# Optimization experiments

Hardware: AMD Instinct MI355X
Metric: run time of the kernel (lower is better)

The kernel has to match this reference:

```python
import jax, jax.numpy as jnp
import numpy as np

N_MEL = 80
ATTN = 512
PRENET = 256
RNN = 1024
B, T = 32, 800


def setup_inputs() -> dict:
    key = jax.random.key(0)
    ks = jax.random.split(key, 10)
    s = lambda fan_in: 1.0 / np.sqrt(fan_in)
    return {
        "memory": jax.random.normal(ks[0], (B, T, ATTN), jnp.float32),
        "y_mels": jax.random.normal(ks[1], (B, T, N_MEL), jnp.float32),
        # Prenet: two bias-free linears with ReLU
        "prenet_w1": jax.random.uniform(ks[2], (PRENET, N_MEL), jnp.float32, -s(N_MEL), s(N_MEL)),
        "prenet_w2": jax.random.uniform(ks[3], (PRENET, PRENET), jnp.float32, -s(PRENET), s(PRENET)),
        # LSTM (1 layer): input dim = PRENET + ATTN = 768, gate order i,f,g,o
        "w_ih": jax.random.uniform(ks[4], (4 * RNN, PRENET + ATTN), jnp.float32, -s(RNN), s(RNN)),
        "w_hh": jax.random.uniform(ks[5], (4 * RNN, RNN), jnp.float32, -s(RNN), s(RNN)),
        "b_ih": jax.random.uniform(ks[6], (4 * RNN,), jnp.float32, -s(RNN), s(RNN)),
        "b_hh": jax.random.uniform(ks[7], (4 * RNN,), jnp.float32, -s(RNN), s(RNN)),
        # Linear projection: (RNN + ATTN) -> N_MEL, with bias
        "proj_w": jax.random.uniform(ks[8], (N_MEL, RNN + ATTN), jnp.float32, -s(RNN + ATTN), s(RNN + ATTN)),
        "proj_b": jax.random.uniform(ks[9], (N_MEL,), jnp.float32, -s(RNN + ATTN), s(RNN + ATTN)),
    }


def _decoder_fwd(memory, y_mels, prenet_w1, prenet_w2, w_ih, w_hh, b_ih, b_hh, proj_w, proj_b):
    b, t, _ = memory.shape
    # teacher-forced previous frames: step j consumes zeros (j=0) or y_mels[:, j-1]
    prev = jnp.concatenate([jnp.zeros((b, 1, N_MEL), memory.dtype), y_mels[:, : t - 1]], axis=1)  # [B,T,80]
    # prenet (eval mode: dropout off; double relu == relu)
    h = jax.nn.relu(jnp.einsum("btm,pm->btp", prev, prenet_w1))
    h = jax.nn.relu(jnp.einsum("btp,qp->btq", h, prenet_w2))  # [B,T,256]
    x = jnp.concatenate([h, memory], axis=-1)  # [B,T,768]
    # precompute input-to-gate contributions for all steps
    gates_in = jnp.einsum("btd,gd->tbg", x, w_ih) + (b_ih + b_hh)  # [T,B,4H]

    def step(carry, g_in):
        hh, cc = carry
        gates = g_in + hh @ w_hh.T  # [B,4H]
        i, f_, g, o = jnp.split(gates, 4, axis=-1)
        cc = jax.nn.sigmoid(f_) * cc + jax.nn.sigmoid(i) * jnp.tanh(g)
        hh = jax.nn.sigmoid(o) * jnp.tanh(cc)
        return (hh, cc), hh

    init = (jnp.zeros((b, RNN), memory.dtype), jnp.zeros((b, RNN), memory.dtype))
    _, hs = jax.lax.scan(step, init, gates_in)  # [T,B,H]
    hs = jnp.transpose(hs, (1, 0, 2))  # [B,T,H]
    out = jnp.concatenate([hs, memory], axis=-1)  # [B,T,H+ATTN]
    mel = jnp.einsum("btd,md->btm", out, proj_w) + proj_b  # [B,T,80]
    return mel.reshape(b, -1, N_MEL)


def reference(memory, y_mels, prenet_w1, prenet_w2, w_ih, w_hh, b_ih, b_hh, proj_w, proj_b):
    return _decoder_fwd(memory, y_mels, prenet_w1, prenet_w2, w_ih, w_hh, b_ih, b_hh, proj_w, proj_b)
```

## Files before the change

kernel.cpp:

```cpp
#include <hip/hip_runtime.h>
#include <hip/hip_bf16.h>

typedef unsigned short u16;
typedef unsigned int u32;
typedef unsigned long long u64;
typedef __attribute__((ext_vector_type(8))) short short8;
typedef __attribute__((ext_vector_type(4))) float f32x4;

#define ROWS 25600

__device__ __forceinline__ u16 f2bf(float f){
  u32 x = __builtin_bit_cast(u32, f);
  u32 r = (x + 0x7FFFu + ((x >> 16) & 1u)) >> 16;
  return (u16)r;
}
__device__ __forceinline__ float bf2f(u16 h){
  return __builtin_bit_cast(float, ((u32)h) << 16);
}
__device__ __forceinline__ float sigf(float x){
  x = fminf(fmaxf(x, -30.f), 30.f);
  return 1.f / (1.f + __expf(-x));
}
__device__ __forceinline__ float tanh_(float x){
  x = fminf(fmaxf(x, -15.f), 15.f);
  float e = __expf(-2.f * x);
  return (1.f - e) / (1.f + e);
}


__global__ void initk(u32* wflags, u32* pflags, u16* hb){
  int i = blockIdx.x * blockDim.x + threadIdx.x;
  int stride = blockDim.x * gridDim.x;
  for (int j = i; j < 64 * 32; j += stride) wflags[j] = 0;
  for (int j = i; j < 192 * 32; j += stride) pflags[j] = 0;
  for (int j = i; j < 2 * 32 * 1024; j += stride) hb[j] = 0;
}

__global__ void sentinel_fill(float* out, int n, float val){
  for (int i = blockIdx.x * blockDim.x + threadIdx.x; i < n;
       i += blockDim.x * gridDim.x)
    out[i] = val;
}

__global__ void prep_prev(const float* __restrict__ ym, u16* __restrict__ prevp){
  int idx = blockIdx.x * blockDim.x + threadIdx.x;
  if (idx >= ROWS * 96) return;
  int r = idx / 96, c = idx - r * 96;
  int b = r / 800, t = r - b * 800;
  float v = 0.f;
  if (c < 80 && t > 0) v = ym[(u64)(b * 800 + (t - 1)) * 80 + c];
  prevp[idx] = f2bf(v);
}

__global__ void prep_w(const float* __restrict__ w1, const float* __restrict__ w2,
                       const float* __restrict__ wih, const float* __restrict__ pw,
                       const float* __restrict__ bih, const float* __restrict__ bhh,
                       const float* __restrict__ whh,
                       u16* __restrict__ w1p, u16* __restrict__ w2b,
                       u16* __restrict__ wihb, u16* __restrict__ projp,
                       float* __restrict__ bsum, u16* __restrict__ whhb){
  int idx = blockIdx.x * blockDim.x + threadIdx.x;
  const int n1 = 256 * 96, n2 = 256 * 256, n3 = 4096 * 768, n4 = 128 * 1536, n5 = 4096;
  const int n6 = 4096 * 1024;
  if (idx < n1){
    int r = idx / 96, c = idx - r * 96;
    w1p[idx] = (c < 80) ? f2bf(w1[r * 80 + c]) : (u16)0;
  } else if ((idx -= n1) < n2){
    w2b[idx] = f2bf(w2[idx]);
  } else if ((idx -= n2) < n3){
    wihb[idx] = f2bf(wih[idx]);
  } else if ((idx -= n3) < n4){
    int r = idx / 1536;
    projp[idx] = (r < 80) ? f2bf(pw[idx]) : (u16)0;
  } else if ((idx -= n4) < n5){
    bsum[idx] = bih[idx] + bhh[idx];
  } else if ((idx -= n5) < n6){
    whhb[idx] = f2bf(whh[idx]);
  }
}


template<int RELU, int OUTF32, int HASBIAS, int AMAP, int SPLIT>
__global__ __launch_bounds__(256, 2) void gemm_tn(
    const u16* __restrict__ A, const float* __restrict__ A2,
    const u16* __restrict__ W, void* __restrict__ Cv,
    const float* __restrict__ bias,
    int M, int K, int lda, int lda2, int ldw, int ldc, int nmax,
    int ksplit, int t0)
{
  __shared__ __align__(16) u16 As[128 * 32];
  __shared__ __align__(16) u16 Ws[128 * 32];
  const int tid = threadIdx.x;
  const int lane = tid & 63;
  const int wv = tid >> 6;
  const int wr = wv & 1, wc = wv >> 1;
  const int mtiles = M >> 7;
  const int ntiles = gridDim.x / mtiles;
  int bm, bn;
  if (mtiles & 7){
    bm = blockIdx.x % mtiles;
    bn = blockIdx.x / mtiles;
  } else {
    int per = 8 * ntiles;
    int g = blockIdx.x / per, rem = blockIdx.x % per;
    bm = g * 8 + (rem & 7);
    bn = rem >> 3;
  }
  const int m0 = bm << 7, n0 = bn << 7;
  const int KT = K >> 5;

  f32x4 acc[4][4] = {};

  const int r0 = tid >> 2, c0 = tid & 3;
  const int r1 = r0 + 64;
  const u16* Wb = W + (u64)n0 * ldw;
  const int ws0 = r0 * 32 + ((c0 ^ ((r0 >> 1) & 3)) << 3);
  const int ws1 = r1 * 32 + ((c0 ^ ((r1 >> 1) & 3)) << 3);

  auto rowmap = [&](int r) -> int {
    int gr = m0 + r;
    if (AMAP) return (gr & 31) * 800 + t0 + (gr >> 5);
    return gr;
  };
  const u64 ab0 = (u64)rowmap(r0) * lda;
  const u64 ab1 = (u64)rowmap(r1) * lda;
  const u64 af0 = SPLIT ? (u64)rowmap(r0) * lda2 : 0;
  const u64 af1 = SPLIT ? (u64)rowmap(r1) * lda2 : 0;

  auto aload = [&](u64 rb, u64 rf, int k) -> uint4 {
    if (SPLIT && k >= ksplit){
      const float* p = A2 + rf + (k - ksplit);
      const float4 a = *(const float4*)p;
      const float4 b = *(const float4*)(p + 4);
      uint4 r;
      r.x = (u32)f2bf(a.x) | ((u32)f2bf(a.y) << 16);
      r.y = (u32)f2bf(a.z) | ((u32)f2bf(a.w) << 16);
      r.z = (u32)f2bf(b.x) | ((u32)f2bf(b.y) << 16);
      r.w = (u32)f2bf(b.z) | ((u32)f2bf(b.w) << 16);
      return r;
    }
    return *(const uint4*)(A + rb + k);
  };

  uint4 ra0 = aload(ab0, af0, c0 * 8);
  uint4 ra1 = aload(ab1, af1, c0 * 8);
  uint4 rw0 = *(const uint4*)(Wb + r0 * ldw + c0 * 8);
  uint4 rw1 = *(const uint4*)(Wb + r1 * ldw + c0 * 8);

  const int r16 = lane & 15, cg = lane >> 4;

  for (int kt = 0; kt < KT; ++kt){
    *(uint4*)&As[ws0] = ra0;
    *(uint4*)&As[ws1] = ra1;
    *(uint4*)&Ws[ws0] = rw0;
    *(uint4*)&Ws[ws1] = rw1;
    __syncthreads();
    if (kt + 1 < KT){
      const int k0 = ((kt + 1) << 5) + c0 * 8;
      ra0 = aload(ab0, af0, k0);
      ra1 = aload(ab1, af1, k0);
      rw0 = *(const uint4*)(Wb + r0 * ldw + k0);
      rw1 = *(const uint4*)(Wb + r1 * ldw + k0);
    }
    short8 af[4], wf[4];
    #pragma unroll
    for (int mt = 0; mt < 4; ++mt){
      const int row = (wr << 6) + (mt << 4) + r16;
      af[mt] = *(const short8*)&As[(row << 5) + ((cg ^ ((row >> 1) & 3)) << 3)];
    }
    #pragma unroll
    for (int nt = 0; nt < 4; ++nt){
      const int row = (wc << 6) + (nt << 4) + r16;
      wf[nt] = *(const short8*)&Ws[(row << 5) + ((cg ^ ((row >> 1) & 3)) << 3)];
    }
    #pragma unroll
    for (int mt = 0; mt < 4; ++mt)
      #pragma unroll
      for (int nt = 0; nt < 4; ++nt)
        acc[mt][nt] = __builtin_amdgcn_mfma_f32_16x16x32_bf16(af[mt], wf[nt], acc[mt][nt], 0, 0, 0);
    __syncthreads();
  }

  #pragma unroll
  for (int nt = 0; nt < 4; ++nt){
    const int gn = n0 + (wc << 6) + (nt << 4) + r16;
    if (gn < nmax){
      float bv = 0.f;
      if (HASBIAS) bv = bias[gn];
      #pragma unroll
      for (int mt = 0; mt < 4; ++mt){
        #pragma unroll
        for (int r = 0; r < 4; ++r){
          const int gm = m0 + (wr << 6) + (mt << 4) + (cg << 2) + r;
          float v = acc[mt][nt][r] + bv;
          if (RELU) v = fmaxf(v, 0.f);
          if (OUTF32) ((float*)Cv)[(u64)gm * ldc + gn] = v;
          else        ((u16*)Cv)[(u64)gm * ldc + gn] = f2bf(v);
        }
      }
    }
  }
}


__shared__ __align__(16) u16 fs_hsm[32 * 1024];
__shared__ __align__(16) float fs_gsm[2048];
__shared__ __align__(16) u16 fs_As[128 * 32];
__shared__ __align__(16) u16 fs_Ws[128 * 32];

__device__ void gemm_tile_512(
    const u16* __restrict__ pn, const float* __restrict__ memory,
    const u16* __restrict__ wihb, const float* __restrict__ bsum,
    u16* __restrict__ slot, int bm, int bn, int t0)
{
  const int tid = threadIdx.x;
  const bool act = (tid < 256);
  const int lane = tid & 63;
  const int wv4 = (tid >> 6) & 3;
  const int wr = wv4 & 1, wc = wv4 >> 1;
  const int m0 = bm << 7, n0 = bn << 7;
  const int KT = 24;

  f32x4 acc[4][4] = {};
  const int r0 = tid >> 2, c0 = tid & 3;
  const int r1 = r0 + 64;
  const u16* Wb = wihb + (u64)n0 * 768;
  const int ws0 = r0 * 32 + ((c0 ^ ((r0 >> 1) & 3)) << 3);
  const int ws1 = r1 * 32 + ((c0 ^ ((r1 >> 1) & 3)) << 3);

  auto rowmap = [&](int r) -> int {
    int gr = m0 + r;
    return (gr & 31) * 800 + t0 + (gr >> 5);
  };
  u64 ab0 = 0, ab1 = 0, af0 = 0, af1 = 0;
  if (act){
    ab0 = (u64)rowmap(r0) * 256;  af0 = (u64)rowmap(r0) * 512;
    ab1 = (u64)rowmap(r1) * 256;  af1 = (u64)rowmap(r1) * 512;
  }
  auto aload = [&](u64 rb, u64 rf, int k) -> uint4 {
    if (k >= 256){
      const float* p = memory + rf + (k - 256);
      const float4 a = *(const float4*)p;
      const float4 b = *(const float4*)(p + 4);
      uint4 r;
      r.x = (u32)f2bf(a.x) | ((u32)f2bf(a.y) << 16);
      r.y = (u32)f2bf(a.z) | ((u32)f2bf(a.w) << 16);
      r.z = (u32)f2bf(b.x) | ((u32)f2bf(b.y) << 16);
      r.w = (u32)f2bf(b.z) | ((u32)f2bf(b.w) << 16);
      return r;
    }
    return *(const uint4*)(pn + rb + k);
  };

  uint4 ra0, ra1, rw0, rw1;
  if (act){
    ra0 = aload(ab0, af0, c0 * 8);
    ra1 = aload(ab1, af1, c0 * 8);
    rw0 = *(const uint4*)(Wb + r0 * 768 + c0 * 8);
    rw1 = *(const uint4*)(Wb + r1 * 768 + c0 * 8);
  }
  const int r16 = lane & 15, cg = lane >> 4;

  for (int kt = 0; kt < KT; ++kt){
    if (act){
      *(uint4*)&fs_As[ws0] = ra0;
      *(uint4*)&fs_As[ws1] = ra1;
      *(uint4*)&fs_Ws[ws0] = rw0;
      *(uint4*)&fs_Ws[ws1] = rw1;
    }
    __syncthreads();
    if (act){
      if (kt + 1 < KT){
        const int k0 = ((kt + 1) << 5) + c0 * 8;
        ra0 = aload(ab0, af0, k0);
        ra1 = aload(ab1, af1, k0);
        rw0 = *(const uint4*)(Wb + r0 * 768 + k0);
        rw1 = *(const uint4*)(Wb + r1 * 768 + k0);
      }
      short8 af[4], wf[4];
      #pragma unroll
      for (int mt = 0; mt < 4; ++mt){
        const int row = (wr << 6) + (mt << 4) + r16;
        af[mt] = *(const short8*)&fs_As[(row << 5) + ((cg ^ ((row >> 1) & 3)) << 3)];
      }
      #pragma unroll
      for (int nt = 0; nt < 4; ++nt){
        const int row = (wc << 6) + (nt << 4) + r16;
        wf[nt] = *(const short8*)&fs_Ws[(row << 5) + ((cg ^ ((row >> 1) & 3)) << 3)];
      }
      #pragma unroll
      for (int mt = 0; mt < 4; ++mt)
        #pragma unroll
        for (int nt = 0; nt < 4; ++nt)
          acc[mt][nt] = __builtin_amdgcn_mfma_f32_16x16x32_bf16(af[mt], wf[nt], acc[mt][nt], 0, 0, 0);
    }
    __syncthreads();
  }

  if (act){
    #pragma unroll
    for (int nt = 0; nt < 4; ++nt){
      const int gn = n0 + (wc << 6) + (nt << 4) + r16;
      const float bv = bsum[gn];
      #pragma unroll
      for (int mt = 0; mt < 4; ++mt){
        #pragma unroll
        for (int r = 0; r < 4; ++r){
          const int gm = m0 + (wr << 6) + (mt << 4) + (cg << 2) + r;
          slot[(u64)gm * 4096 + gn] = f2bf(acc[mt][nt][r] + bv);
        }
      }
    }
  }
}

__global__ __launch_bounds__(512, 1) void fused(
    const u16* __restrict__ whhb, const u16* __restrict__ pn,
    const float* __restrict__ memory, const u16* __restrict__ wihb,
    const float* __restrict__ bsum, u16* __restrict__ ring,
    u16* __restrict__ hb, u16* __restrict__ hs,
    u32* wflags, u32* pflags, int CT, int nchunks)
{
  const int tid = threadIdx.x;
  const int lane = tid & 63;
  const int wv = tid >> 6;
  const u64 deadline = __builtin_amdgcn_s_memrealtime() + 100000000ull;

  if (blockIdx.x >= 64){
    const int p = blockIdx.x - 64;
    for (int c = 0; c < nchunks; ++c){
      const int t0 = c * CT;
      const int steps = (800 - t0 < CT) ? (800 - t0) : CT;
      if (c >= 2){
        if (wv == 0){
          const u32 need = (u32)((c - 1) * CT);
          u32 it = 0;
          while (1){
            u32 v = __hip_atomic_load(&wflags[lane << 5], __ATOMIC_RELAXED,
                                      __HIP_MEMORY_SCOPE_AGENT);
            if (__all((int)(v >= need))) break;
            __builtin_amdgcn_s_sleep(8);
            if (((++it) & 15u) == 0u &&
                __builtin_amdgcn_s_memrealtime() > deadline) break;
          }
        }
        __syncthreads();
      }
      const int mt = (steps * 32) >> 7;
      const int TPC = mt * 32;
      u16* slot = ring + (u64)(c & 1) * ((u64)CT << 17);
      for (int tau = p; tau < TPC; tau += 192){
        gemm_tile_512(pn, memory, wihb, bsum, slot, tau % mt, tau / mt, t0);
      }
      __syncthreads();
      if (wv == 0){
        __builtin_amdgcn_fence(__ATOMIC_RELEASE, "agent");
        if (tid == 0)
          __hip_atomic_store(&pflags[p << 5], (u32)(c + 1), __ATOMIC_RELAXED,
                             __HIP_MEMORY_SCOPE_AGENT);
      }
    }
    return;
  }

  const int gate = wv & 3, mh = wv >> 2;
  const int u0 = blockIdx.x << 4;
  const int r16 = lane & 15, cg = lane >> 4;

  short8 wf[32];
  {
    const u16* wrow = whhb + (u64)((gate << 10) + u0 + r16) * 1024 + (cg << 3);
    #pragma unroll
    for (int kk = 0; kk < 32; ++kk)
      wf[kk] = *(const short8*)(wrow + (kk << 5));
  }

  const int pb = tid >> 4, pu = tid & 15;
  float ccell = 0.f;
  const int arow = (mh << 4) + r16;
  const u16* abase = &fs_hsm[arow << 10];
  const int aswz = (arow & 7) << 3;

  int c = 0, i = 0;
  for (int t = 0; t < 800; ++t, ++i){
    if (i == CT){ c++; i = 0; }
    const bool boundary = (i == 0);
    const u16* gslot = ring + (u64)(c & 1) * ((u64)CT << 17);
    const u64 gb = ((u64)i * 32 + pb) * 4096 + u0 + pu;
    const int cur = t & 1;

    u16 gv0 = 0, gv1 = 0, gv2 = 0, gv3 = 0;
    if (!boundary){
      gv0 = gslot[gb];        gv1 = gslot[gb + 1024];
      gv2 = gslot[gb + 2048]; gv3 = gslot[gb + 3072];
    }
    if (boundary || t > 0){
      if (wv == 0){
        if (boundary){
          const u32 need = (u32)(c + 1);
          u32 it = 0;
          while (1){
            u32 a = __hip_atomic_load(&pflags[lane << 5], __ATOMIC_RELAXED,
                                      __HIP_MEMORY_SCOPE_AGENT);
            u32 b = __hip_atomic_load(&pflags[(lane + 64) << 5], __ATOMIC_RELAXED,
                                      __HIP_MEMORY_SCOPE_AGENT);
            u32 d = __hip_atomic_load(&pflags[(lane + 128) << 5], __ATOMIC_RELAXED,
                                      __HIP_MEMORY_SCOPE_AGENT);
            u32 m = a < b ? a : b; m = m < d ? m : d;
            if (__all((int)(m >= need))) break;
            if (((++it) & 15u) == 0u &&
                __builtin_amdgcn_s_memrealtime() > deadline) break;
          }
        }
        if (t > 0){
          u32 it = 0;
          while (1){
            u32 v = __hip_atomic_load(&wflags[lane << 5], __ATOMIC_RELAXED,
                                      __HIP_MEMORY_SCOPE_AGENT);
            if (__all((int)(v >= (u32)t))) break;
            if (((++it) & 15u) == 0u &&
                __builtin_amdgcn_s_memrealtime() > deadline) break;
          }
        }
        __builtin_amdgcn_fence(__ATOMIC_ACQUIRE, "agent");
      }
      __syncthreads();
    }
    if (boundary){
      gv0 = gslot[gb];        gv1 = gslot[gb + 1024];
      gv2 = gslot[gb + 2048]; gv3 = gslot[gb + 3072];
    }
    {
      const u16* hsrc = hb + cur * 32768;
      uint4 hr[8];
      #pragma unroll
      for (int j = 0; j < 8; ++j) hr[j] = *(const uint4*)(hsrc + (((j << 9) + tid) << 3));
      #pragma unroll
      for (int j = 0; j < 8; ++j){
        const int ci = (j << 9) + tid;
        const int row = ci >> 7, k16 = ci & 127;
        *(uint4*)&fs_hsm[(row << 10) + ((k16 ^ (row & 7)) << 3)] = hr[j];
      }
    }
    __syncthreads();
    f32x4 acc = {};
    #pragma unroll
    for (int kk = 0; kk < 32; ++kk){
      const int k16 = (kk << 2) + cg;
      const short8 af = *(const short8*)&abase[((k16 << 3) ^ aswz)];
      acc = __builtin_amdgcn_mfma_f32_16x16x32_bf16(af, wf[kk], acc, 0, 0, 0);
    }
    #pragma unroll
    for (int r = 0; r < 4; ++r){
      const int m = (mh << 4) + (cg << 2) + r;
      fs_gsm[(gate << 9) + (m << 4) + r16] = acc[r];
    }
    __syncthreads();
    {
      const int o = (pb << 4) + pu;
      const float gi = fs_gsm[o]        + bf2f(gv0);
      const float gf = fs_gsm[512 + o]  + bf2f(gv1);
      const float gg = fs_gsm[1024 + o] + bf2f(gv2);
      const float go = fs_gsm[1536 + o] + bf2f(gv3);
      ccell = sigf(gf) * ccell + sigf(gi) * tanh_(gg);
      const float h = sigf(go) * tanh_(ccell);
      const u16 hbits = f2bf(h);
      hs[(((u64)pb * 800 + t) << 10) + u0 + pu] = hbits;
      const u32 other = (u32)(u16)__shfl_xor((int)(u32)hbits, 1);
      if ((tid & 1) == 0){
        const u32 w = ((u32)hbits) | (other << 16);
        u32* dst = (u32*)(void*)hb + ((cur ^ 1) * 16384 + (pb << 9) + (u0 >> 1) + (pu >> 1));
        __hip_atomic_store(dst, w, __ATOMIC_RELAXED, __HIP_MEMORY_SCOPE_AGENT);
      }
    }
    __syncthreads();
    if (tid == 0)
      __hip_atomic_store(&wflags[blockIdx.x << 5], (u32)(t + 1), __ATOMIC_RELAXED,
                         __HIP_MEMORY_SCOPE_AGENT);
  }
}


extern "C" void kernel_launch(void* const* d_in, const int* in_sizes, int n_in,
                              void* d_out, int out_size, void* d_ws, size_t ws_size,
                              hipStream_t stream){
  const float* memory = (const float*)d_in[0];
  const float* ymels  = (const float*)d_in[1];
  const float* w1     = (const float*)d_in[2];
  const float* w2     = (const float*)d_in[3];
  const float* wih    = (const float*)d_in[4];
  const float* whh    = (const float*)d_in[5];
  const float* bih    = (const float*)d_in[6];
  const float* bhh    = (const float*)d_in[7];
  const float* pw     = (const float*)d_in[8];
  const float* pbias  = (const float*)d_in[9];
  float* out = (float*)d_out;

  char* ws = (char*)d_ws;
  u64 off = 0;
  auto alloc = [&](u64 bytes) -> void* {
    void* p = ws + off;
    off += (bytes + 255) & ~255ull;
    return p;
  };
  u16* hs    = (u16*)alloc((u64)ROWS * 1024 * 2);
  u16* pn    = (u16*)alloc((u64)ROWS * 256 * 2);
  u16* wihb  = (u16*)alloc((u64)4096 * 768 * 2);
  u16* whhb  = (u16*)alloc((u64)4096 * 1024 * 2);
  u16* w1p   = (u16*)alloc(256 * 96 * 2);
  u16* w2b   = (u16*)alloc(256 * 256 * 2);
  u16* projp = (u16*)alloc(128 * 1536 * 2);
  float* bsum = (float*)alloc(4096 * 4);
  u16* hb    = (u16*)alloc(2 * 32768 * 2);
  u32* wflags = (u32*)alloc(64 * 32 * 4);
  u32* pflags = (u32*)alloc(192 * 32 * 4);
  u16* prevp = hs;
  u16* h1b   = hs + (8u << 20);

  int CT = 0;
  u16* ring = (u16*)(ws + off);
  if (ws_size > off){
    u64 avail = ws_size - off;
    CT = (int)(avail / (2ull * 32 * 4096 * 2));
    CT &= ~3;
    if (CT > 64) CT = 64;
  }
  if (CT < 8){
    float val = 1.0e6f + 10.0f * (float)(ws_size >> 20);
    sentinel_fill<<<256, 256, 0, stream>>>(out, out_size, val);
    return;
  }
  const int nchunks = (800 + CT - 1) / CT;

  initk<<<64, 256, 0, stream>>>(wflags, pflags, hb);
  prep_prev<<<(ROWS * 96) / 256, 256, 0, stream>>>(ymels, prevp);
  prep_w<<<(256*96 + 256*256 + 4096*768 + 128*1536 + 4096 + 4096*1024 + 255) / 256,
           256, 0, stream>>>(
      w1, w2, wih, pw, bih, bhh, whh, w1p, w2b, wihb, projp, bsum, whhb);

  gemm_tn<1,0,0,0,0><<<200 * 2, 256, 0, stream>>>(prevp, nullptr, w1p, h1b, nullptr,
      ROWS, 96, 96, 0, 96, 256, 256, 0, 0);
  gemm_tn<1,0,0,0,0><<<200 * 2, 256, 0, stream>>>(h1b, nullptr, w2b, pn, nullptr,
      ROWS, 256, 256, 0, 256, 256, 256, 0, 0);

  fused<<<256, 512, 0, stream>>>(whhb, pn, memory, wihb, bsum, ring, hb, hs,
                                 wflags, pflags, CT, nchunks);

  gemm_tn<0,1,1,0,1><<<200 * 1, 256, 0, stream>>>(hs, memory, projp, out, pbias,
      ROWS, 1536, 1024, 512, 1536, 80, 80, 1024, 0);
}
```

Before: 3.010 ms.

## Replace per-step barrier with LDS counter signaling and relaxed atomic h exchange

In the recurrent LSTM loop, the trailing __syncthreads plus single-thread flag store is replaced by a per-wave vmcnt wait and an LDS atomic counter; the last wave to arrive publishes the step flag. The acquire fence is now issued only at chunk boundaries, and the hidden state is read back with 64-bit relaxed atomic loads and written as packed 64-bit atomic stores. The gate ring chunk size is capped at 32 instead of 64. The aim is to cut barrier and fence latency on the serial critical path, at the cost of relying on relaxed atomics for cross-block visibility without an acquire fence on every step.

```diff
diff --git a/kernel.cpp b/kernel.cpp
--- a/kernel.cpp
+++ b/kernel.cpp
@@ -207,6 +207,7 @@
 __shared__ __align__(16) float fs_gsm[2048];
 __shared__ __align__(16) u16 fs_As[128 * 32];
 __shared__ __align__(16) u16 fs_Ws[128 * 32];
+__shared__ u32 fs_done;
 
 __device__ void gemm_tile_512(
     const u16* __restrict__ pn, const float* __restrict__ memory,
@@ -367,6 +368,8 @@
   const int u0 = blockIdx.x << 4;
   const int r16 = lane & 15, cg = lane >> 4;
 
+  if (tid == 0) fs_done = 0;
+
   short8 wf[32];
   {
     const u16* wrow = whhb + (u64)((gate << 10) + u0 + r16) * 1024 + (cg << 3);
@@ -374,6 +377,7 @@
     for (int kk = 0; kk < 32; ++kk)
       wf[kk] = *(const short8*)(wrow + (kk << 5));
   }
+  __syncthreads();
 
   const int pb = tid >> 4, pu = tid & 15;
   float ccell = 0.f;
@@ -422,7 +426,8 @@
                 __builtin_amdgcn_s_memrealtime() > deadline) break;
           }
         }
-        __builtin_amdgcn_fence(__ATOMIC_ACQUIRE, "agent");
+        if (boundary)
+          __builtin_amdgcn_fence(__ATOMIC_ACQUIRE, "agent");
       }
       __syncthreads();
     }
@@ -431,15 +436,19 @@
       gv2 = gslot[gb + 2048]; gv3 = gslot[gb + 3072];
     }
     {
-      const u16* hsrc = hb + cur * 32768;
-      uint4 hr[8];
-      #pragma unroll
-      for (int j = 0; j < 8; ++j) hr[j] = *(const uint4*)(hsrc + (((j << 9) + tid) << 3));
-      #pragma unroll
-      for (int j = 0; j < 8; ++j){
+      const u64* hsrc = (const u64*)(void*)(hb + cur * 32768);
+      u64 hr[16];
+      #pragma unroll
+      for (int j = 0; j < 16; ++j)
+        hr[j] = __hip_atomic_load(&hsrc[(j << 9) + tid], __ATOMIC_RELAXED,
+                                  __HIP_MEMORY_SCOPE_AGENT);
+      #pragma unroll
+      for (int j = 0; j < 16; ++j){
         const int ci = (j << 9) + tid;
-        const int row = ci >> 7, k16 = ci & 127;
-        *(uint4*)&fs_hsm[(row << 10) + ((k16 ^ (row & 7)) << 3)] = hr[j];
+        const int row = ci >> 8;
+        const int col8 = ci & 255;
+        const int k16 = col8 >> 1, lo = col8 & 1;
+        *(u64*)((char*)fs_hsm + (row << 11) + ((k16 ^ (row & 7)) << 4) + (lo << 3)) = hr[j];
       }
     }
     __syncthreads();
@@ -466,17 +475,21 @@
       const float h = sigf(go) * tanh_(ccell);
       const u16 hbits = f2bf(h);
       hs[(((u64)pb * 800 + t) << 10) + u0 + pu] = hbits;
-      const u32 other = (u32)(u16)__shfl_xor((int)(u32)hbits, 1);
-      if ((tid & 1) == 0){
-        const u32 w = ((u32)hbits) | (other << 16);
-        u32* dst = (u32*)(void*)hb + ((cur ^ 1) * 16384 + (pb << 9) + (u0 >> 1) + (pu >> 1));
+      const u32 w1 = ((u32)hbits) | (((u32)(u16)__shfl_xor((int)(u32)hbits, 1)) << 16);
+      const u32 w2 = (u32)__shfl_xor((int)w1, 2);
+      if ((tid & 3) == 0){
+        const u64 w = ((u64)w1) | (((u64)w2) << 32);
+        u64* dst = (u64*)(void*)hb + ((cur ^ 1) * 8192 + (pb << 8) + (u0 >> 2) + (pu >> 2));
         __hip_atomic_store(dst, w, __ATOMIC_RELAXED, __HIP_MEMORY_SCOPE_AGENT);
       }
     }
-    __syncthreads();
-    if (tid == 0)
-      __hip_atomic_store(&wflags[blockIdx.x << 5], (u32)(t + 1), __ATOMIC_RELAXED,
-                         __HIP_MEMORY_SCOPE_AGENT);
+    asm volatile("s_waitcnt vmcnt(0)" ::: "memory");
+    if (lane == 0){
+      u32 old = atomicAdd(&fs_done, 1u);
+      if (old == (u32)(8 * t + 7))
+        __hip_atomic_store(&wflags[blockIdx.x << 5], (u32)(t + 1), __ATOMIC_RELAXED,
+                           __HIP_MEMORY_SCOPE_AGENT);
+    }
   }
 }
 
@@ -523,7 +536,7 @@
     u64 avail = ws_size - off;
     CT = (int)(avail / (2ull * 32 * 4096 * 2));
     CT &= ~3;
-    if (CT > 64) CT = 64;
+    if (CT > 32) CT = 32;
   }
   if (CT < 8){
     float val = 1.0e6f + 10.0f * (float)(ws_size >> 20);
```

After: 3.729 ms. +23.9%, slower.
